# Kernel tuning notes

Measured on AMD Instinct MI355X. Metric: run time of the kernel, lower is better.

Reference implementation:

```python
import jax, jax.numpy as jnp
import numpy as np

EPS = 1e-5  # BatchNorm eps (torch default)


def _norm_adj(adj):
    # DenseGCNConv: add self-loops, symmetric degree normalization
    N = adj.shape[-1]
    adj = adj + jnp.eye(N, dtype=adj.dtype)
    d = jnp.clip(adj.sum(-1), 1.0, None) ** -0.5
    return d[..., :, None] * adj * d[..., None, :]


def _gcn(x, adj_norm, W, b):
    return jnp.einsum('bij,bjf->bif', adj_norm, x @ W) + b


def _batchnorm(h, gamma, beta):
    # torch BatchNorm1d in training mode over flattened (B*N, C)
    B, N, C = h.shape
    hf = h.reshape(B * N, C)
    mu = hf.mean(0)
    var = hf.var(0)  # biased, as used for normalization
    out = (hf - mu) * jax.lax.rsqrt(var + EPS) * gamma + beta
    return out.reshape(B, N, C)


def setup_inputs() -> dict:
    key = jax.random.key(0)
    ks = jax.random.split(key, 24)
    B, N, F, H, D = 4, 256, 6, 128, 256
    s = 0.05
    a = jax.random.uniform(ks[1], (B, N, N), dtype=jnp.float32)
    adj = ((a + jnp.swapaxes(a, 1, 2)) / 2 < 0.1).astype(jnp.float32)  # sparse symmetric adjacency
    return {
        'x': jax.random.normal(ks[0], (B, N, F), dtype=jnp.float32),
        'adj': adj,
        'W1': jax.random.normal(ks[2], (F, H)) * s, 'b1': jnp.zeros((H,)),
        'W2': jax.random.normal(ks[3], (H, H)) * s, 'b2': jnp.zeros((H,)),
        'W3': jax.random.normal(ks[4], (H, D)) * s, 'b3': jnp.zeros((D,)),
        'g1': jnp.ones((H,)), 'beta1': jnp.zeros((H,)),
        'g2': jnp.ones((H,)), 'beta2': jnp.zeros((H,)),
        'e1w': jax.random.normal(ks[5], (2 * D, H)) * s, 'e1b': jnp.zeros((H,)),
        'e2w': jax.random.normal(ks[6], (H, H // 2)) * s, 'e2b': jnp.zeros((H // 2,)),
        'e3w': jax.random.normal(ks[7], (H // 2, 1)) * s, 'e3b': jnp.zeros((1,)),
        'f1w': jax.random.normal(ks[8], (D, H)) * s, 'f1b': jnp.zeros((H,)),
        'f2w': jax.random.normal(ks[9], (H, H)) * s, 'f2b': jnp.zeros((H,)),
        'f3w': jax.random.normal(ks[10], (H, F)) * s, 'f3b': jnp.zeros((F,)),
    }


def reference(x, adj, W1, b1, W2, b2, W3, b3, g1, beta1, g2, beta2,
              e1w, e1b, e2w, e2b, e3w, e3b, f1w, f1b, f2w, f2b, f3w, f3b):
    adj_norm = _norm_adj(adj)
    h = jax.nn.relu(_batchnorm(_gcn(x, adj_norm, W1, b1), g1, beta1))
    h = jax.nn.relu(_batchnorm(_gcn(h, adj_norm, W2, b2), g2, beta2))
    h = jax.nn.relu(_gcn(h, adj_norm, W3, b3))  # [B,N,D]
    D = h.shape[-1]
    # AdjacencyDecoder: Linear(cat(h_i,h_j)) == h_i@e1w[:D] + h_j@e1w[D:] (fused form, same math)
    hi = h @ e1w[:D]   # [B,N,H]
    hj = h @ e1w[D:]   # [B,N,H]
    p = jax.nn.relu(hi[:, :, None, :] + hj[:, None, :, :] + e1b)  # [B,N,N,H]
    p = jax.nn.relu(p @ e2w + e2b)                                 # [B,N,N,H/2]
    logits = (p @ e3w + e3b)[..., 0]                               # [B,N,N]
    logits = (logits + jnp.swapaxes(logits, 1, 2)) / 2
    adj_pred = jax.nn.sigmoid(logits)
    # FeatureDecoder
    f = jax.nn.relu(h @ f1w + f1b)
    f = jax.nn.relu(f @ f2w + f2b)
    feat_pred = f @ f3w + f3b
    return adj_pred, feat_pred
```

## Files before the change

kernel.cpp:

```cpp
#include <hip/hip_runtime.h>


typedef float v4f __attribute__((ext_vector_type(4)));
typedef short v8s __attribute__((ext_vector_type(8)));

__device__ __forceinline__ unsigned short f2bs(float f) {
    union { float f; unsigned int u; } v;
    v.f = f;
    return (unsigned short)((v.u + 0x7fffu + ((v.u >> 16) & 1u)) >> 16);
}

__global__ void k_pre(const float* x, const float* W1, const float* adj,
                      const float* e2w, float* buf, float* dg,
                      unsigned short* bfr_g, float* st) {
    __shared__ float ss[256];
    int blk = blockIdx.x, tid = threadIdx.x;
    if (blk < 512) {
        int idx = blk * 256 + tid;
        int m = idx >> 7, n = idx & 127;
        float s = 0.f;
        for (int k = 0; k < 6; k++) s += x[m * 6 + k] * W1[k * 128 + n];
        buf[idx] = s;
    } else if (blk < 768) {
        int row = (blk - 512) * 4 + (tid >> 6);
        int lane = tid & 63;
        const float* ap = adj + (long)row * 256;
        ss[tid] = ap[lane] + ap[lane + 64] + ap[lane + 128] + ap[lane + 192];
        __syncthreads();
        for (int o = 32; o > 0; o >>= 1) {
            if (lane < o) ss[tid] += ss[tid + o];
            __syncthreads();
        }
        if (lane == 0) {
            float t = ss[tid] + 1.f;
            if (t < 1.f) t = 1.f;
            dg[row] = rsqrtf(t);
        }
    } else {
        for (int s = tid; s < 8192; s += 256) {
            int k = s >> 6, n = s & 63;
            int kc = k >> 5, q = (k & 31) >> 3, t = k & 7;
            int nt = n >> 4, c2 = n & 15;
            bfr_g[(((nt * 4 + kc) * 64) + q * 16 + c2) * 8 + t] = f2bs(e2w[s]);
        }
        st[tid] = 0.f;
        st[256 + tid] = 0.f;
    }
}

__device__ void dev_tile(int t, const float* A, const float* B, const float* bias,
                         const float* dgA, float* anOut,
                         const float* stat, const float* g, const float* beta,
                         float* ostat, float* C,
                         int K, int N, int relu,
                         int sA, int sB, int sC, int tiles_n, int tiles_m,
                         float* smem) {
    float* As = smem;
    float* Bs = smem + 4352;
    int tid = threadIdx.x;
    int n2 = tid & 15, ml = tid >> 4;
    int bx = t % tiles_n;
    int tmp = t / tiles_n;
    int by = tmp % tiles_m;
    int bz = tmp / tiles_m;
    int m0 = by * 16, n0 = bx * 32;
    const float* Ab = A + (long)bz * sA;
    const float* Bb = B + (long)bz * sB;
    float* Cb = C + (long)bz * sC;
    const float* dgb = (dgA != 0) ? (dgA + bz * 256) : 0;

    int kk = tid & 15, mm = tid >> 4;
    int nb = tid & 31, kb = tid >> 5;
    float di = (dgA != 0) ? dgb[m0 + mm] : 0.f;
    for (int ka = 0; ka < K; ka += 16) {
        int kg = ka + kk;
        float v = Ab[(long)(m0 + mm) * K + kg];
        if (dgA != 0) {
            if (m0 + mm == kg) v += 1.f;
            v = di * v * dgb[kg];
            if (anOut != 0 && bx == 0)
                anOut[bz * 65536 + (m0 + mm) * 256 + kg] = v;
        } else if (stat != 0) {
            float mu = stat[kg] * (1.f / 1024.f);
            float vr = stat[128 + kg] * (1.f / 1024.f) - mu * mu;
            float sc = rsqrtf(vr + 1e-5f) * g[kg];
            v = (v - mu) * sc + beta[kg];
            if (v < 0.f) v = 0.f;
        }
        As[kg * 17 + mm] = v;
        int kg2 = ka + kb;
        Bs[kg2 * 32 + nb] = Bb[(long)kg2 * N + n0 + nb];
        kg2 = ka + kb + 8;
        Bs[kg2 * 32 + nb] = Bb[(long)kg2 * N + n0 + nb];
    }
    __syncthreads();
    float c0 = 0.f, c1 = 0.f;
    #pragma unroll 8
    for (int q = 0; q < K; q++) {
        float a = As[q * 17 + ml];
        c0 += a * Bs[q * 32 + n2 * 2];
        c1 += a * Bs[q * 32 + n2 * 2 + 1];
    }
    int mRow = m0 + ml, nn = n0 + n2 * 2;
    if (bias != 0) { c0 += bias[nn]; c1 += bias[nn + 1]; }
    if (relu) {
        if (c0 < 0.f) c0 = 0.f;
        if (c1 < 0.f) c1 = 0.f;
    }
    Cb[(long)mRow * N + nn] = c0;
    Cb[(long)mRow * N + nn + 1] = c1;

    if (ostat != 0) {
        float* sred = smem;
        float* qred = smem + 544;
        __syncthreads();
        sred[(n2 * 2) * 17 + ml] = c0;
        sred[(n2 * 2 + 1) * 17 + ml] = c1;
        qred[(n2 * 2) * 17 + ml] = c0 * c0;
        qred[(n2 * 2 + 1) * 17 + ml] = c1 * c1;
        __syncthreads();
        if (tid < 32) {
            float s = 0.f, q = 0.f;
            for (int u = 0; u < 16; u++) {
                s += sred[tid * 17 + u];
                q += qred[tid * 17 + u];
            }
            atomicAdd(&ostat[n0 + tid], s);
            atomicAdd(&ostat[128 + n0 + tid], q);
        }
    }
}

__global__ void k_tgemm(const float* A, const float* B, const float* bias,
                        const float* dgA, float* anOut,
                        const float* stat, const float* g, const float* beta,
                        float* ostat, float* C,
                        int K, int N, int relu,
                        int sA, int sB, int sC, int tiles_n, int tiles_m) {
    __shared__ float smem[12544];
    dev_tile(blockIdx.x, A, B, bias, dgA, anOut, stat, g, beta, ostat, C,
             K, N, relu, sA, sB, sC, tiles_n, tiles_m, smem);
}

__global__ void k_g67(const float* hb, const float* e1w, float* hi,
                      const float* f1w, const float* f1b, float* f1) {
    __shared__ float smem[12544];
    int t = blockIdx.x;
    if (t < 512) {
        dev_tile(t, hb, e1w, 0, 0, 0, 0, 0, 0, 0, hi,
                 256, 128, 0, 0, 32768, 131072, 4, 64, smem);
    } else {
        dev_tile(t - 512, hb, f1w, f1b, 0, 0, 0, 0, 0, 0, f1,
                 256, 128, 1, 0, 0, 0, 4, 64, smem);
    }
}

__global__ void k_decf(const float* hi, const float* hj, const float* e1b,
                       const unsigned short* bfr_g, const float* e2b,
                       const float* e3w, const float* e3b,
                       const float* f1, const float* f2w, const float* f2b_,
                       const float* f3w, const float* f3b,
                       float* lg, float* out) {
    __shared__ float smem[4608];
    int tid = threadIdx.x;
    int blk = blockIdx.x;
    if (blk < 1024) {
        float* red = smem;
        float* pre_sh = smem + 4352;
        int lane = tid & 63, wv = tid >> 6;
        int col = lane & 15, quad = lane >> 4;
        int bi = blk, b = bi >> 8;
        if (tid < 128) pre_sh[tid] = hi[bi * 128 + tid] + e1b[tid];
        __syncthreads();
        float e2bv[4], e3wv[4];
        for (int nt = 0; nt < 4; nt++) {
            e2bv[nt] = e2b[nt * 16 + col];
            e3wv[nt] = e3w[nt * 16 + col];
        }
        const float* hjb = hj + b * 32768;
        #pragma unroll 1
        for (int ms = 0; ms < 4; ms++) {
            v4f acc[4];
            for (int nt = 0; nt < 4; nt++) {
                v4f z = {0.f, 0.f, 0.f, 0.f};
                acc[nt] = z;
            }
            int j = wv * 64 + ms * 16 + col;
            const float* rowp = hjb + j * 128 + quad * 8;
            #pragma unroll 1
            for (int kc = 0; kc < 4; kc++) {
                const float* pp = pre_sh + kc * 32 + quad * 8;
                const float* hp = rowp + kc * 32;
                v8s af;
                #pragma unroll
                for (int t = 0; t < 8; t++) {
                    float p = pp[t] + hp[t];
                    p = (p > 0.f) ? p : 0.f;
                    af[t] = (short)f2bs(p);
                }
                #pragma unroll
                for (int nt = 0; nt < 4; nt++) {
                    v8s bf = *(const v8s*)&bfr_g[(((nt * 4 + kc) * 64) + lane) * 8];
                    acc[nt] = __builtin_amdgcn_mfma_f32_16x16x32_bf16(
                        af, bf, acc[nt], 0, 0, 0);
                }
            }
            #pragma unroll
            for (int r = 0; r < 4; r++) {
                float s = 0.f;
                #pragma unroll
                for (int nt = 0; nt < 4; nt++) {
                    float v = acc[nt][r] + e2bv[nt];
                    if (v > 0.f) s += v * e3wv[nt];
                }
                red[(wv * 64 + ms * 16 + quad * 4 + r) * 17 + col] = s;
            }
        }
        __syncthreads();
        float s = e3b[0];
        for (int c = 0; c < 16; c++) s += red[tid * 17 + c];
        lg[bi * 256 + tid] = s;
    } else {
        float* f2row = smem;
        int r0 = (blk - 1024) * 4;
        for (int p = 0; p < 2; p++) {
            int idx = tid + p * 256;
            int r = r0 + (idx >> 7), n = idx & 127;
            float s = f2b_[n];
            const float* f1r = f1 + (long)r * 128;
            for (int k = 0; k < 128; k++) s += f1r[k] * f2w[k * 128 + n];
            if (s < 0.f) s = 0.f;
            f2row[idx] = s;
        }
        __syncthreads();
        if (tid < 24) {
            int r = tid / 6, c = tid % 6;
            float s = f3b[c];
            const float* fr = f2row + r * 128;
            for (int k = 0; k < 128; k++) s += fr[k] * f3w[k * 6 + c];
            out[262144 + (r0 + r) * 6 + c] = s;
        }
    }
}

__global__ void k_symsig(const float* lg, float* out) {
    __shared__ float Ta[32 * 33];
    __shared__ float Tb[32 * 33];
    int tid = threadIdx.x;
    int b = blockIdx.x / 36;
    int t = blockIdx.x % 36;
    int ti = 0, rem = t;
    while (rem >= 8 - ti) { rem -= 8 - ti; ti++; }
    int tj = ti + rem;
    int i0 = ti * 32, j0 = tj * 32;
    const float* lgb = lg + b * 65536;
    for (int p = 0; p < 4; p++) {
        int idx = p * 256 + tid;
        int r = idx >> 5, c = idx & 31;
        Ta[r * 33 + c] = lgb[(i0 + r) * 256 + j0 + c];
        Tb[r * 33 + c] = lgb[(j0 + r) * 256 + i0 + c];
    }
    __syncthreads();
    float* ob = out + b * 65536;
    for (int p = 0; p < 4; p++) {
        int idx = p * 256 + tid;
        int r = idx >> 5, c = idx & 31;
        float v1 = 0.5f * (Ta[r * 33 + c] + Tb[c * 33 + r]);
        ob[(i0 + r) * 256 + j0 + c] = 1.f / (1.f + expf(-v1));
        float v2 = 0.5f * (Tb[r * 33 + c] + Ta[c * 33 + r]);
        ob[(j0 + r) * 256 + i0 + c] = 1.f / (1.f + expf(-v2));
    }
}

extern "C" void kernel_launch(void* const* d_in, const int* in_sizes, int n_in,
                              void* d_out, int out_size, void* d_ws, size_t ws_size,
                              hipStream_t stream) {
    const float* x   = (const float*)d_in[0];
    const float* adj = (const float*)d_in[1];
    const float* W1  = (const float*)d_in[2];
    const float* b1  = (const float*)d_in[3];
    const float* W2  = (const float*)d_in[4];
    const float* b2  = (const float*)d_in[5];
    const float* W3  = (const float*)d_in[6];
    const float* b3  = (const float*)d_in[7];
    const float* g1  = (const float*)d_in[8];
    const float* be1 = (const float*)d_in[9];
    const float* g2  = (const float*)d_in[10];
    const float* be2 = (const float*)d_in[11];
    const float* e1w = (const float*)d_in[12];
    const float* e1b = (const float*)d_in[13];
    const float* e2w = (const float*)d_in[14];
    const float* e2b = (const float*)d_in[15];
    const float* e3w = (const float*)d_in[16];
    const float* e3b = (const float*)d_in[17];
    const float* f1w = (const float*)d_in[18];
    const float* f1b = (const float*)d_in[19];
    const float* f2w = (const float*)d_in[20];
    const float* f2b_ = (const float*)d_in[21];
    const float* f3w = (const float*)d_in[22];
    const float* f3b = (const float*)d_in[23];

    float* out = (float*)d_out;

    if (ws_size < (size_t)1600000 * 4) {
        hipMemsetAsync(d_out, 0x60, 4096, stream);
        return;
    }
    float* ws = (float*)d_ws;
    float* st1 = ws;
    float* st2 = ws + 256;
    float* dg  = ws + 512;
    unsigned short* bfr_g = (unsigned short*)(ws + 1536);
    float* An  = ws + 5632;
    float* buf = An + 262144;
    float* hb  = buf + 262144;
    float* lg  = hb + 262144;
    float* h1  = lg + 262144;
    float* h2  = h1 + 131072;
    float* hi  = h2 + 131072;
    float* hj  = hi + 131072;

    k_pre<<<769, 256, 0, stream>>>(x, W1, adj, e2w, buf, dg, bfr_g, st1);
    k_tgemm<<<256, 256, 0, stream>>>(adj, buf, b1, dg, An, 0, 0, 0, st1, h1,
                                     256, 128, 0, 65536, 32768, 32768, 4, 16);
    k_tgemm<<<256, 256, 0, stream>>>(h1, W2, 0, 0, 0, st1, g1, be1, 0, buf,
                                     128, 128, 0, 0, 0, 0, 4, 64);
    k_tgemm<<<256, 256, 0, stream>>>(An, buf, b2, 0, 0, 0, 0, 0, st2, h2,
                                     256, 128, 0, 65536, 32768, 32768, 4, 16);
    k_tgemm<<<512, 256, 0, stream>>>(h2, W3, 0, 0, 0, st2, g2, be2, 0, buf,
                                     128, 256, 0, 0, 0, 0, 8, 64);
    k_tgemm<<<512, 256, 0, stream>>>(An, buf, b3, 0, 0, 0, 0, 0, 0, hb,
                                     256, 256, 1, 65536, 65536, 65536, 8, 16);
    k_g67<<<768, 256, 0, stream>>>(hb, e1w, hi, f1w, f1b, h1);
    k_decf<<<1280, 256, 0, stream>>>(hi, hj, e1b, bfr_g, e2b, e3w, e3b,
                                     h1, f2w, f2b_, f3w, f3b, lg, out);
    k_symsig<<<144, 256, 0, stream>>>(lg, out);
}
```

Measured before the change: 217.7 us.

## Fuse logit symmetrization and sigmoid into decoder by computing both orientations

```diff
diff --git a/kernel.cpp b/kernel.cpp
--- a/kernel.cpp
+++ b/kernel.cpp
@@ -155,71 +155,89 @@
     }
 }
 
+__device__ float dec_half(const float* rows, const float* pre_sh,
+                          const unsigned short* bfr_g,
+                          const float* e2bv, const float* e3wv, float e3bv,
+                          float* red) {
+    int tid = threadIdx.x;
+    int lane = tid & 63, wv = tid >> 6;
+    int col = lane & 15, quad = lane >> 4;
+    __syncthreads();
+    #pragma unroll 1
+    for (int ms = 0; ms < 4; ms++) {
+        v4f acc[4];
+        for (int nt = 0; nt < 4; nt++) {
+            v4f z = {0.f, 0.f, 0.f, 0.f};
+            acc[nt] = z;
+        }
+        int j = wv * 64 + ms * 16 + col;
+        const float* rowp = rows + j * 128 + quad * 8;
+        #pragma unroll 1
+        for (int kc = 0; kc < 4; kc++) {
+            const float* pp = pre_sh + kc * 32 + quad * 8;
+            const float* hp = rowp + kc * 32;
+            v8s af;
+            #pragma unroll
+            for (int t = 0; t < 8; t++) {
+                float p = pp[t] + hp[t];
+                p = (p > 0.f) ? p : 0.f;
+                af[t] = (short)f2bs(p);
+            }
+            #pragma unroll
+            for (int nt = 0; nt < 4; nt++) {
+                v8s bf = *(const v8s*)&bfr_g[(((nt * 4 + kc) * 64) + lane) * 8];
+                acc[nt] = __builtin_amdgcn_mfma_f32_16x16x32_bf16(
+                    af, bf, acc[nt], 0, 0, 0);
+            }
+        }
+        #pragma unroll
+        for (int r = 0; r < 4; r++) {
+            float s = 0.f;
+            #pragma unroll
+            for (int nt = 0; nt < 4; nt++) {
+                float v = acc[nt][r] + e2bv[nt];
+                if (v > 0.f) s += v * e3wv[nt];
+            }
+            red[(wv * 64 + ms * 16 + quad * 4 + r) * 17 + col] = s;
+        }
+    }
+    __syncthreads();
+    float s = e3bv;
+    for (int c = 0; c < 16; c++) s += red[tid * 17 + c];
+    return s;
+}
+
 __global__ void k_decf(const float* hi, const float* hj, const float* e1b,
                        const unsigned short* bfr_g, const float* e2b,
                        const float* e3w, const float* e3b,
                        const float* f1, const float* f2w, const float* f2b_,
                        const float* f3w, const float* f3b,
-                       float* lg, float* out) {
+                       float* out) {
     __shared__ float smem[4608];
     int tid = threadIdx.x;
     int blk = blockIdx.x;
     if (blk < 1024) {
-        float* red = smem;
-        float* pre_sh = smem + 4352;
-        int lane = tid & 63, wv = tid >> 6;
-        int col = lane & 15, quad = lane >> 4;
+        float* red  = smem;
+        float* pre1 = smem + 4352;
+        float* pre2 = smem + 4480;
+        int lane = tid & 63;
+        int col = lane & 15;
         int bi = blk, b = bi >> 8;
-        if (tid < 128) pre_sh[tid] = hi[bi * 128 + tid] + e1b[tid];
+        if (tid < 128) {
+            pre1[tid] = hi[bi * 128 + tid] + e1b[tid];
+            pre2[tid] = hj[bi * 128 + tid] + e1b[tid];
+        }
         __syncthreads();
         float e2bv[4], e3wv[4];
         for (int nt = 0; nt < 4; nt++) {
             e2bv[nt] = e2b[nt * 16 + col];
             e3wv[nt] = e3w[nt * 16 + col];
         }
-        const float* hjb = hj + b * 32768;
-        #pragma unroll 1
-        for (int ms = 0; ms < 4; ms++) {
-            v4f acc[4];
-            for (int nt = 0; nt < 4; nt++) {
-                v4f z = {0.f, 0.f, 0.f, 0.f};
-                acc[nt] = z;
-            }
-            int j = wv * 64 + ms * 16 + col;
-            const float* rowp = hjb + j * 128 + quad * 8;
-            #pragma unroll 1
-            for (int kc = 0; kc < 4; kc++) {
-                const float* pp = pre_sh + kc * 32 + quad * 8;
-                const float* hp = rowp + kc * 32;
-                v8s af;
-                #pragma unroll
-                for (int t = 0; t < 8; t++) {
-                    float p = pp[t] + hp[t];
-                    p = (p > 0.f) ? p : 0.f;
-                    af[t] = (short)f2bs(p);
-                }
-                #pragma unroll
-                for (int nt = 0; nt < 4; nt++) {
-                    v8s bf = *(const v8s*)&bfr_g[(((nt * 4 + kc) * 64) + lane) * 8];
-                    acc[nt] = __builtin_amdgcn_mfma_f32_16x16x32_bf16(
-                        af, bf, acc[nt], 0, 0, 0);
-                }
-            }
-            #pragma unroll
-            for (int r = 0; r < 4; r++) {
-                float s = 0.f;
-                #pragma unroll
-                for (int nt = 0; nt < 4; nt++) {
-                    float v = acc[nt][r] + e2bv[nt];
-                    if (v > 0.f) s += v * e3wv[nt];
-                }
-                red[(wv * 64 + ms * 16 + quad * 4 + r) * 17 + col] = s;
-            }
-        }
-        __syncthreads();
-        float s = e3b[0];
-        for (int c = 0; c < 16; c++) s += red[tid * 17 + c];
-        lg[bi * 256 + tid] = s;
+        float e3bv = e3b[0];
+        float l1 = dec_half(hj + b * 32768, pre1, bfr_g, e2bv, e3wv, e3bv, red);
+        float l2 = dec_half(hi + b * 32768, pre2, bfr_g, e2bv, e3wv, e3bv, red);
+        float v = 0.5f * (l1 + l2);
+        out[bi * 256 + tid] = 1.f / (1.f + expf(-v));
     } else {
         float* f2row = smem;
         int r0 = (blk - 1024) * 4;
@@ -240,35 +258,6 @@
             for (int k = 0; k < 128; k++) s += fr[k] * f3w[k * 6 + c];
             out[262144 + (r0 + r) * 6 + c] = s;
         }
-    }
-}
-
-__global__ void k_symsig(const float* lg, float* out) {
-    __shared__ float Ta[32 * 33];
-    __shared__ float Tb[32 * 33];
-    int tid = threadIdx.x;
-    int b = blockIdx.x / 36;
-    int t = blockIdx.x % 36;
-    int ti = 0, rem = t;
-    while (rem >= 8 - ti) { rem -= 8 - ti; ti++; }
-    int tj = ti + rem;
-    int i0 = ti * 32, j0 = tj * 32;
-    const float* lgb = lg + b * 65536;
-    for (int p = 0; p < 4; p++) {
-        int idx = p * 256 + tid;
-        int r = idx >> 5, c = idx & 31;
-        Ta[r * 33 + c] = lgb[(i0 + r) * 256 + j0 + c];
-        Tb[r * 33 + c] = lgb[(j0 + r) * 256 + i0 + c];
-    }
-    __syncthreads();
-    float* ob = out + b * 65536;
-    for (int p = 0; p < 4; p++) {
-        int idx = p * 256 + tid;
-        int r = idx >> 5, c = idx & 31;
-        float v1 = 0.5f * (Ta[r * 33 + c] + Tb[c * 33 + r]);
-        ob[(i0 + r) * 256 + j0 + c] = 1.f / (1.f + expf(-v1));
-        float v2 = 0.5f * (Tb[r * 33 + c] + Ta[c * 33 + r]);
-        ob[(j0 + r) * 256 + i0 + c] = 1.f / (1.f + expf(-v2));
     }
 }
 
@@ -302,7 +291,7 @@
 
     float* out = (float*)d_out;
 
-    if (ws_size < (size_t)1600000 * 4) {
+    if (ws_size < (size_t)1400000 * 4) {
         hipMemsetAsync(d_out, 0x60, 4096, stream);
         return;
     }
@@ -314,8 +303,7 @@
     float* An  = ws + 5632;
     float* buf = An + 262144;
     float* hb  = buf + 262144;
-    float* lg  = hb + 262144;
-    float* h1  = lg + 262144;
+    float* h1  = hb + 262144;
     float* h2  = h1 + 131072;
     float* hi  = h2 + 131072;
     float* hj  = hi + 131072;
@@ -333,6 +321,5 @@
                                      256, 256, 1, 65536, 65536, 65536, 8, 16);
     k_g67<<<768, 256, 0, stream>>>(hb, e1w, hi, f1w, f1b, h1);
     k_decf<<<1280, 256, 0, stream>>>(hi, hj, e1b, bfr_g, e2b, e3w, e3b,
-                                     h1, f2w, f2b_, f3w, f3b, lg, out);
-    k_symsig<<<144, 256, 0, stream>>>(lg, out);
-}
+                                     h1, f2w, f2b_, f3w, f3b, out);
+}
```

After: 234.2 us. 1.08x slower.

## Fuse all stages into one persistent kernel with software grid barriers

Applied to the files above, without the earlier changes.

```diff
diff --git a/kernel.cpp b/kernel.cpp
--- a/kernel.cpp
+++ b/kernel.cpp
@@ -3,6 +3,8 @@
 
 typedef float v4f __attribute__((ext_vector_type(4)));
 typedef short v8s __attribute__((ext_vector_type(8)));
+
+#define NBLK 768
 
 __device__ __forceinline__ unsigned short f2bs(float f) {
     union { float f; unsigned int u; } v;
@@ -10,42 +12,30 @@
     return (unsigned short)((v.u + 0x7fffu + ((v.u >> 16) & 1u)) >> 16);
 }
 
-__global__ void k_pre(const float* x, const float* W1, const float* adj,
-                      const float* e2w, float* buf, float* dg,
-                      unsigned short* bfr_g, float* st) {
-    __shared__ float ss[256];
-    int blk = blockIdx.x, tid = threadIdx.x;
-    if (blk < 512) {
-        int idx = blk * 256 + tid;
-        int m = idx >> 7, n = idx & 127;
-        float s = 0.f;
-        for (int k = 0; k < 6; k++) s += x[m * 6 + k] * W1[k * 128 + n];
-        buf[idx] = s;
-    } else if (blk < 768) {
-        int row = (blk - 512) * 4 + (tid >> 6);
-        int lane = tid & 63;
-        const float* ap = adj + (long)row * 256;
-        ss[tid] = ap[lane] + ap[lane + 64] + ap[lane + 128] + ap[lane + 192];
-        __syncthreads();
-        for (int o = 32; o > 0; o >>= 1) {
-            if (lane < o) ss[tid] += ss[tid + o];
-            __syncthreads();
-        }
-        if (lane == 0) {
-            float t = ss[tid] + 1.f;
-            if (t < 1.f) t = 1.f;
-            dg[row] = rsqrtf(t);
-        }
-    } else {
-        for (int s = tid; s < 8192; s += 256) {
-            int k = s >> 6, n = s & 63;
-            int kc = k >> 5, q = (k & 31) >> 3, t = k & 7;
-            int nt = n >> 4, c2 = n & 15;
-            bfr_g[(((nt * 4 + kc) * 64) + q * 16 + c2) * 8 + t] = f2bs(e2w[s]);
-        }
-        st[tid] = 0.f;
-        st[256 + tid] = 0.f;
-    }
+__device__ void gbar(int* ctrl) {
+    __syncthreads();
+    if (threadIdx.x == 0) {
+        volatile int* genp = (volatile int*)(ctrl + 576 + (blockIdx.x & 7) * 32);
+        int g = *genp;
+        __threadfence();
+        int p = blockIdx.x & 15;
+        const int per = NBLK / 16;
+        if (atomicAdd(ctrl + p * 32, 1) == per - 1) {
+            if (atomicAdd(ctrl + 512, per) == NBLK - per) {
+                for (int q = 0; q < 16; q++) atomicExch(ctrl + q * 32, 0);
+                atomicExch(ctrl + 512, 0);
+                __threadfence();
+                for (int q = 0; q < 8; q++) atomicAdd(ctrl + 576 + q * 32, 1);
+            }
+        }
+        long it = 0;
+        while (*genp == g) {
+            __builtin_amdgcn_s_sleep(16);
+            if (++it > 2000000L) break;
+        }
+    }
+    __syncthreads();
+    __threadfence();
 }
 
 __device__ void dev_tile(int t, const float* A, const float* B, const float* bias,
@@ -56,7 +46,7 @@
                          int sA, int sB, int sC, int tiles_n, int tiles_m,
                          float* smem) {
     float* As = smem;
-    float* Bs = smem + 4352;
+    float* Bs = smem + 272;
     int tid = threadIdx.x;
     int n2 = tid & 15, ml = tid >> 4;
     int bx = t % tiles_n;
@@ -68,12 +58,11 @@
     const float* Bb = B + (long)bz * sB;
     float* Cb = C + (long)bz * sC;
     const float* dgb = (dgA != 0) ? (dgA + bz * 256) : 0;
-
     int kk = tid & 15, mm = tid >> 4;
-    int nb = tid & 31, kb = tid >> 5;
     float di = (dgA != 0) ? dgb[m0 + mm] : 0.f;
-    for (int ka = 0; ka < K; ka += 16) {
-        int kg = ka + kk;
+    float c0 = 0.f, c1 = 0.f;
+    for (int k0 = 0; k0 < K; k0 += 16) {
+        int kg = k0 + kk;
         float v = Ab[(long)(m0 + mm) * K + kg];
         if (dgA != 0) {
             if (m0 + mm == kg) v += 1.f;
@@ -87,19 +76,20 @@
             v = (v - mu) * sc + beta[kg];
             if (v < 0.f) v = 0.f;
         }
-        As[kg * 17 + mm] = v;
-        int kg2 = ka + kb;
-        Bs[kg2 * 32 + nb] = Bb[(long)kg2 * N + n0 + nb];
-        kg2 = ka + kb + 8;
-        Bs[kg2 * 32 + nb] = Bb[(long)kg2 * N + n0 + nb];
-    }
-    __syncthreads();
-    float c0 = 0.f, c1 = 0.f;
-    #pragma unroll 8
-    for (int q = 0; q < K; q++) {
-        float a = As[q * 17 + ml];
-        c0 += a * Bs[q * 32 + n2 * 2];
-        c1 += a * Bs[q * 32 + n2 * 2 + 1];
+        As[kk * 17 + mm] = v;
+        int nn2 = tid & 31, kk2 = tid >> 5;
+        Bs[kk2 * 33 + nn2] = Bb[(long)(k0 + kk2) * N + n0 + nn2];
+        int idx = tid + 256;
+        nn2 = idx & 31; kk2 = idx >> 5;
+        Bs[kk2 * 33 + nn2] = Bb[(long)(k0 + kk2) * N + n0 + nn2];
+        __syncthreads();
+        #pragma unroll
+        for (int q = 0; q < 16; q++) {
+            float a = As[q * 17 + ml];
+            c0 += a * Bs[q * 33 + n2 * 2];
+            c1 += a * Bs[q * 33 + n2 * 2 + 1];
+        }
+        __syncthreads();
     }
     int mRow = m0 + ml, nn = n0 + n2 * 2;
     if (bias != 0) { c0 += bias[nn]; c1 += bias[nn + 1]; }
@@ -111,8 +101,8 @@
     Cb[(long)mRow * N + nn + 1] = c1;
 
     if (ostat != 0) {
-        float* sred = smem;
-        float* qred = smem + 544;
+        float* sred = smem + 800;
+        float* qred = smem + 1344;
         __syncthreads();
         sred[(n2 * 2) * 17 + ml] = c0;
         sred[(n2 * 2 + 1) * 17 + ml] = c1;
@@ -131,187 +121,27 @@
     }
 }
 
-__global__ void k_tgemm(const float* A, const float* B, const float* bias,
-                        const float* dgA, float* anOut,
-                        const float* stat, const float* g, const float* beta,
-                        float* ostat, float* C,
-                        int K, int N, int relu,
-                        int sA, int sB, int sC, int tiles_n, int tiles_m) {
-    __shared__ float smem[12544];
-    dev_tile(blockIdx.x, A, B, bias, dgA, anOut, stat, g, beta, ostat, C,
-             K, N, relu, sA, sB, sC, tiles_n, tiles_m, smem);
-}
-
-__global__ void k_g67(const float* hb, const float* e1w, float* hi,
-                      const float* f1w, const float* f1b, float* f1) {
-    __shared__ float smem[12544];
-    int t = blockIdx.x;
-    if (t < 512) {
-        dev_tile(t, hb, e1w, 0, 0, 0, 0, 0, 0, 0, hi,
-                 256, 128, 0, 0, 32768, 131072, 4, 64, smem);
-    } else {
-        dev_tile(t - 512, hb, f1w, f1b, 0, 0, 0, 0, 0, 0, f1,
-                 256, 128, 1, 0, 0, 0, 4, 64, smem);
-    }
-}
-
-__global__ void k_decf(const float* hi, const float* hj, const float* e1b,
-                       const unsigned short* bfr_g, const float* e2b,
-                       const float* e3w, const float* e3b,
-                       const float* f1, const float* f2w, const float* f2b_,
-                       const float* f3w, const float* f3b,
-                       float* lg, float* out) {
+__global__ void k_all(const float* x, const float* adj,
+                      const float* W1, const float* b1,
+                      const float* W2, const float* b2,
+                      const float* W3, const float* b3,
+                      const float* g1, const float* be1,
+                      const float* g2, const float* be2,
+                      const float* e1w, const float* e1b,
+                      const float* e2w, const float* e2b,
+                      const float* e3w, const float* e3b,
+                      const float* f1w, const float* f1b,
+                      const float* f2w, const float* f2b_,
+                      const float* f3w, const float* f3b,
+                      float* ws, float* out) {
     __shared__ float smem[4608];
-    int tid = threadIdx.x;
-    int blk = blockIdx.x;
-    if (blk < 1024) {
-        float* red = smem;
-        float* pre_sh = smem + 4352;
-        int lane = tid & 63, wv = tid >> 6;
-        int col = lane & 15, quad = lane >> 4;
-        int bi = blk, b = bi >> 8;
-        if (tid < 128) pre_sh[tid] = hi[bi * 128 + tid] + e1b[tid];
-        __syncthreads();
-        float e2bv[4], e3wv[4];
-        for (int nt = 0; nt < 4; nt++) {
-            e2bv[nt] = e2b[nt * 16 + col];
-            e3wv[nt] = e3w[nt * 16 + col];
-        }
-        const float* hjb = hj + b * 32768;
-        #pragma unroll 1
-        for (int ms = 0; ms < 4; ms++) {
-            v4f acc[4];
-            for (int nt = 0; nt < 4; nt++) {
-                v4f z = {0.f, 0.f, 0.f, 0.f};
-                acc[nt] = z;
-            }
-            int j = wv * 64 + ms * 16 + col;
-            const float* rowp = hjb + j * 128 + quad * 8;
-            #pragma unroll 1
-            for (int kc = 0; kc < 4; kc++) {
-                const float* pp = pre_sh + kc * 32 + quad * 8;
-                const float* hp = rowp + kc * 32;
-                v8s af;
-                #pragma unroll
-                for (int t = 0; t < 8; t++) {
-                    float p = pp[t] + hp[t];
-                    p = (p > 0.f) ? p : 0.f;
-                    af[t] = (short)f2bs(p);
-                }
-                #pragma unroll
-                for (int nt = 0; nt < 4; nt++) {
-                    v8s bf = *(const v8s*)&bfr_g[(((nt * 4 + kc) * 64) + lane) * 8];
-                    acc[nt] = __builtin_amdgcn_mfma_f32_16x16x32_bf16(
-                        af, bf, acc[nt], 0, 0, 0);
-                }
-            }
-            #pragma unroll
-            for (int r = 0; r < 4; r++) {
-                float s = 0.f;
-                #pragma unroll
-                for (int nt = 0; nt < 4; nt++) {
-                    float v = acc[nt][r] + e2bv[nt];
-                    if (v > 0.f) s += v * e3wv[nt];
-                }
-                red[(wv * 64 + ms * 16 + quad * 4 + r) * 17 + col] = s;
-            }
-        }
-        __syncthreads();
-        float s = e3b[0];
-        for (int c = 0; c < 16; c++) s += red[tid * 17 + c];
-        lg[bi * 256 + tid] = s;
-    } else {
-        float* f2row = smem;
-        int r0 = (blk - 1024) * 4;
-        for (int p = 0; p < 2; p++) {
-            int idx = tid + p * 256;
-            int r = r0 + (idx >> 7), n = idx & 127;
-            float s = f2b_[n];
-            const float* f1r = f1 + (long)r * 128;
-            for (int k = 0; k < 128; k++) s += f1r[k] * f2w[k * 128 + n];
-            if (s < 0.f) s = 0.f;
-            f2row[idx] = s;
-        }
-        __syncthreads();
-        if (tid < 24) {
-            int r = tid / 6, c = tid % 6;
-            float s = f3b[c];
-            const float* fr = f2row + r * 128;
-            for (int k = 0; k < 128; k++) s += fr[k] * f3w[k * 6 + c];
-            out[262144 + (r0 + r) * 6 + c] = s;
-        }
-    }
-}
-
-__global__ void k_symsig(const float* lg, float* out) {
-    __shared__ float Ta[32 * 33];
-    __shared__ float Tb[32 * 33];
-    int tid = threadIdx.x;
-    int b = blockIdx.x / 36;
-    int t = blockIdx.x % 36;
-    int ti = 0, rem = t;
-    while (rem >= 8 - ti) { rem -= 8 - ti; ti++; }
-    int tj = ti + rem;
-    int i0 = ti * 32, j0 = tj * 32;
-    const float* lgb = lg + b * 65536;
-    for (int p = 0; p < 4; p++) {
-        int idx = p * 256 + tid;
-        int r = idx >> 5, c = idx & 31;
-        Ta[r * 33 + c] = lgb[(i0 + r) * 256 + j0 + c];
-        Tb[r * 33 + c] = lgb[(j0 + r) * 256 + i0 + c];
-    }
-    __syncthreads();
-    float* ob = out + b * 65536;
-    for (int p = 0; p < 4; p++) {
-        int idx = p * 256 + tid;
-        int r = idx >> 5, c = idx & 31;
-        float v1 = 0.5f * (Ta[r * 33 + c] + Tb[c * 33 + r]);
-        ob[(i0 + r) * 256 + j0 + c] = 1.f / (1.f + expf(-v1));
-        float v2 = 0.5f * (Tb[r * 33 + c] + Ta[c * 33 + r]);
-        ob[(j0 + r) * 256 + i0 + c] = 1.f / (1.f + expf(-v2));
-    }
-}
-
-extern "C" void kernel_launch(void* const* d_in, const int* in_sizes, int n_in,
-                              void* d_out, int out_size, void* d_ws, size_t ws_size,
-                              hipStream_t stream) {
-    const float* x   = (const float*)d_in[0];
-    const float* adj = (const float*)d_in[1];
-    const float* W1  = (const float*)d_in[2];
-    const float* b1  = (const float*)d_in[3];
-    const float* W2  = (const float*)d_in[4];
-    const float* b2  = (const float*)d_in[5];
-    const float* W3  = (const float*)d_in[6];
-    const float* b3  = (const float*)d_in[7];
-    const float* g1  = (const float*)d_in[8];
-    const float* be1 = (const float*)d_in[9];
-    const float* g2  = (const float*)d_in[10];
-    const float* be2 = (const float*)d_in[11];
-    const float* e1w = (const float*)d_in[12];
-    const float* e1b = (const float*)d_in[13];
-    const float* e2w = (const float*)d_in[14];
-    const float* e2b = (const float*)d_in[15];
-    const float* e3w = (const float*)d_in[16];
-    const float* e3b = (const float*)d_in[17];
-    const float* f1w = (const float*)d_in[18];
-    const float* f1b = (const float*)d_in[19];
-    const float* f2w = (const float*)d_in[20];
-    const float* f2b_ = (const float*)d_in[21];
-    const float* f3w = (const float*)d_in[22];
-    const float* f3b = (const float*)d_in[23];
-
-    float* out = (float*)d_out;
-
-    if (ws_size < (size_t)1600000 * 4) {
-        hipMemsetAsync(d_out, 0x60, 4096, stream);
-        return;
-    }
-    float* ws = (float*)d_ws;
-    float* st1 = ws;
-    float* st2 = ws + 256;
-    float* dg  = ws + 512;
-    unsigned short* bfr_g = (unsigned short*)(ws + 1536);
-    float* An  = ws + 5632;
+
+    int* ctrl = (int*)ws;
+    float* st1 = ws + 1024;
+    float* st2 = ws + 1280;
+    float* dg  = ws + 1536;
+    unsigned short* bfr_g = (unsigned short*)(ws + 2560);
+    float* An  = ws + 6656;
     float* buf = An + 262144;
     float* hb  = buf + 262144;
     float* lg  = hb + 262144;
@@ -320,19 +150,209 @@
     float* hi  = h2 + 131072;
     float* hj  = hi + 131072;
 
-    k_pre<<<769, 256, 0, stream>>>(x, W1, adj, e2w, buf, dg, bfr_g, st1);
-    k_tgemm<<<256, 256, 0, stream>>>(adj, buf, b1, dg, An, 0, 0, 0, st1, h1,
-                                     256, 128, 0, 65536, 32768, 32768, 4, 16);
-    k_tgemm<<<256, 256, 0, stream>>>(h1, W2, 0, 0, 0, st1, g1, be1, 0, buf,
-                                     128, 128, 0, 0, 0, 0, 4, 64);
-    k_tgemm<<<256, 256, 0, stream>>>(An, buf, b2, 0, 0, 0, 0, 0, st2, h2,
-                                     256, 128, 0, 65536, 32768, 32768, 4, 16);
-    k_tgemm<<<512, 256, 0, stream>>>(h2, W3, 0, 0, 0, st2, g2, be2, 0, buf,
-                                     128, 256, 0, 0, 0, 0, 8, 64);
-    k_tgemm<<<512, 256, 0, stream>>>(An, buf, b3, 0, 0, 0, 0, 0, 0, hb,
-                                     256, 256, 1, 65536, 65536, 65536, 8, 16);
-    k_g67<<<768, 256, 0, stream>>>(hb, e1w, hi, f1w, f1b, h1);
-    k_decf<<<1280, 256, 0, stream>>>(hi, hj, e1b, bfr_g, e2b, e3w, e3b,
-                                     h1, f2w, f2b_, f3w, f3b, lg, out);
-    k_symsig<<<144, 256, 0, stream>>>(lg, out);
-}
+    int tid = threadIdx.x;
+    int blk = blockIdx.x;
+
+    if (blk < 512) {
+        int idx = blk * 256 + tid;
+        int m = idx >> 7, n = idx & 127;
+        float s = 0.f;
+        for (int k = 0; k < 6; k++) s += x[m * 6 + k] * W1[k * 128 + n];
+        buf[idx] = s;
+        if (blk < 32) {
+            int s2 = blk * 256 + tid;
+            int k = s2 >> 6, n2 = s2 & 63;
+            int kc = k >> 5, q = (k & 31) >> 3, t = k & 7;
+            int nt = n2 >> 4, c2 = n2 & 15;
+            bfr_g[(((nt * 4 + kc) * 64) + q * 16 + c2) * 8 + t] = f2bs(e2w[s2]);
+        } else if (blk == 32) {
+            st1[tid] = 0.f;
+            st1[256 + tid] = 0.f;
+        }
+    } else {
+        float* ss = smem;
+        int row = (blk - 512) * 4 + (tid >> 6);
+        int lane = tid & 63;
+        const float* ap = adj + (long)row * 256;
+        ss[tid] = ap[lane] + ap[lane + 64] + ap[lane + 128] + ap[lane + 192];
+        __syncthreads();
+        for (int o = 32; o > 0; o >>= 1) {
+            if (lane < o) ss[tid] += ss[tid + o];
+            __syncthreads();
+        }
+        if (lane == 0) {
+            float t = ss[tid] + 1.f;
+            if (t < 1.f) t = 1.f;
+            dg[row] = rsqrtf(t);
+        }
+    }
+    gbar(ctrl);
+
+    if (blk < 256)
+        dev_tile(blk, adj, buf, b1, dg, An, 0, 0, 0, st1, h1,
+                 256, 128, 0, 65536, 32768, 32768, 4, 16, smem);
+    gbar(ctrl);
+
+    if (blk < 256)
+        dev_tile(blk, h1, W2, 0, 0, 0, st1, g1, be1, 0, buf,
+                 128, 128, 0, 0, 0, 0, 4, 64, smem);
+    gbar(ctrl);
+
+    if (blk < 256)
+        dev_tile(blk, An, buf, b2, 0, 0, 0, 0, 0, st2, h2,
+                 256, 128, 0, 65536, 32768, 32768, 4, 16, smem);
+    gbar(ctrl);
+
+    if (blk < 512)
+        dev_tile(blk, h2, W3, 0, 0, 0, st2, g2, be2, 0, buf,
+                 128, 256, 0, 0, 0, 0, 8, 64, smem);
+    gbar(ctrl);
+
+    if (blk < 512)
+        dev_tile(blk, An, buf, b3, 0, 0, 0, 0, 0, 0, hb,
+                 256, 256, 1, 65536, 65536, 65536, 8, 16, smem);
+    gbar(ctrl);
+
+    if (blk < 512)
+        dev_tile(blk, hb, e1w, 0, 0, 0, 0, 0, 0, 0, hi,
+                 256, 128, 0, 0, 32768, 131072, 4, 64, smem);
+    else
+        dev_tile(blk - 512, hb, f1w, f1b, 0, 0, 0, 0, 0, 0, h1,
+                 256, 128, 1, 0, 0, 0, 4, 64, smem);
+    gbar(ctrl);
+
+    for (int u = blk; u < 1280; u += NBLK) {
+        __syncthreads();
+        if (u < 1024) {
+            float* red = smem;
+            float* pre_sh = smem + 4352;
+            int lane = tid & 63, wv = tid >> 6;
+            int col = lane & 15, quad = lane >> 4;
+            int bi = u, b = bi >> 8;
+            if (tid < 128) pre_sh[tid] = hi[bi * 128 + tid] + e1b[tid];
+            __syncthreads();
+            float e2bv[4], e3wv[4];
+            for (int nt = 0; nt < 4; nt++) {
+                e2bv[nt] = e2b[nt * 16 + col];
+                e3wv[nt] = e3w[nt * 16 + col];
+            }
+            const float* hjb = hj + b * 32768;
+            #pragma unroll 1
+            for (int ms = 0; ms < 4; ms++) {
+                v4f acc[4];
+                for (int nt = 0; nt < 4; nt++) {
+                    v4f z = {0.f, 0.f, 0.f, 0.f};
+                    acc[nt] = z;
+                }
+                int j = wv * 64 + ms * 16 + col;
+                const float* rowp = hjb + j * 128 + quad * 8;
+                #pragma unroll 1
+                for (int kc = 0; kc < 4; kc++) {
+                    const float* pp = pre_sh + kc * 32 + quad * 8;
+                    const float* hp = rowp + kc * 32;
+                    v8s af;
+                    #pragma unroll
+                    for (int t = 0; t < 8; t++) {
+                        float p = pp[t] + hp[t];
+                        p = (p > 0.f) ? p : 0.f;
+                        af[t] = (short)f2bs(p);
+                    }
+                    #pragma unroll
+                    for (int nt = 0; nt < 4; nt++) {
+                        v8s bf = *(const v8s*)&bfr_g[(((nt * 4 + kc) * 64) + lane) * 8];
+                        acc[nt] = __builtin_amdgcn_mfma_f32_16x16x32_bf16(
+                            af, bf, acc[nt], 0, 0, 0);
+                    }
+                }
+                #pragma unroll
+                for (int r = 0; r < 4; r++) {
+                    float s = 0.f;
+                    #pragma unroll
+                    for (int nt = 0; nt < 4; nt++) {
+                        float v = acc[nt][r] + e2bv[nt];
+                        if (v > 0.f) s += v * e3wv[nt];
+                    }
+                    red[(wv * 64 + ms * 16 + quad * 4 + r) * 17 + col] = s;
+                }
+            }
+            __syncthreads();
+            float s = e3b[0];
+            for (int c = 0; c < 16; c++) s += red[tid * 17 + c];
+            lg[bi * 256 + tid] = s;
+        } else {
+            float* f2row = smem;
+            int r0 = (u - 1024) * 4;
+            for (int p = 0; p < 2; p++) {
+                int idx = tid + p * 256;
+                int r = r0 + (idx >> 7), n = idx & 127;
+                float s = f2b_[n];
+                const float* f1r = h1 + (long)r * 128;
+                for (int k = 0; k < 128; k++) s += f1r[k] * f2w[k * 128 + n];
+                if (s < 0.f) s = 0.f;
+                f2row[idx] = s;
+            }
+            __syncthreads();
+            if (tid < 24) {
+                int r = tid / 6, c = tid % 6;
+                float s = f3b[c];
+                const float* fr = f2row + r * 128;
+                for (int k = 0; k < 128; k++) s += fr[k] * f3w[k * 6 + c];
+                out[262144 + (r0 + r) * 6 + c] = s;
+            }
+        }
+    }
+    gbar(ctrl);
+
+    if (blk < 144) {
+        float* Ta = smem;
+        float* Tb = smem + 1056;
+        int b = blk / 36;
+        int t = blk % 36;
+        int ti = 0, rem = t;
+        while (rem >= 8 - ti) { rem -= 8 - ti; ti++; }
+        int tj = ti + rem;
+        int i0 = ti * 32, j0 = tj * 32;
+        const float* lgb = lg + b * 65536;
+        for (int p = 0; p < 4; p++) {
+            int idx = p * 256 + tid;
+            int r = idx >> 5, c = idx & 31;
+            Ta[r * 33 + c] = lgb[(i0 + r) * 256 + j0 + c];
+            Tb[r * 33 + c] = lgb[(j0 + r) * 256 + i0 + c];
+        }
+        __syncthreads();
+        float* ob = out + b * 65536;
+        for (int p = 0; p < 4; p++) {
+            int idx = p * 256 + tid;
+            int r = idx >> 5, c = idx & 31;
+            float v1 = 0.5f * (Ta[r * 33 + c] + Tb[c * 33 + r]);
+            ob[(i0 + r) * 256 + j0 + c] = 1.f / (1.f + expf(-v1));
+            float v2 = 0.5f * (Tb[r * 33 + c] + Ta[c * 33 + r]);
+            ob[(j0 + r) * 256 + i0 + c] = 1.f / (1.f + expf(-v2));
+        }
+    }
+}
+
+extern "C" void kernel_launch(void* const* d_in, const int* in_sizes, int n_in,
+                              void* d_out, int out_size, void* d_ws, size_t ws_size,
+                              hipStream_t stream) {
+    if (ws_size < (size_t)1600000 * 4) {
+        hipMemsetAsync(d_out, 0x60, 4096, stream);
+        return;
+    }
+    hipMemsetAsync(d_ws, 0, 4096, stream);
+
+    k_all<<<NBLK, 256, 0, stream>>>(
+        (const float*)d_in[0],  (const float*)d_in[1],
+        (const float*)d_in[2],  (const float*)d_in[3],
+        (const float*)d_in[4],  (const float*)d_in[5],
+        (const float*)d_in[6],  (const float*)d_in[7],
+        (const float*)d_in[8],  (const float*)d_in[9],
+        (const float*)d_in[10], (const float*)d_in[11],
+        (const float*)d_in[12], (const float*)d_in[13],
+        (const float*)d_in[14], (const float*)d_in[15],
+        (const float*)d_in[16], (const float*)d_in[17],
+        (const float*)d_in[18], (const float*)d_in[19],
+        (const float*)d_in[20], (const float*)d_in[21],
+        (const float*)d_in[22], (const float*)d_in[23],
+        (float*)d_ws, (float*)d_out);
+}
```

After: 668.2 us. 207% more time.
